# Optimization experiments

Hardware: AMD Instinct MI355X
Metric: run time of the kernel (lower is better)

Reference implementation:

```python
import jax, jax.numpy as jnp
import numpy as np

LAMBDA_COORD = 5.0
LAMBDA_NOOBJ = 0.5
EPS = 1e-16


def setup_inputs() -> dict:
    key = jax.random.key(0)
    k1, k2, k3 = jax.random.split(key, 3)
    B, HW, C = 64, 6400, 85  # 80x80 grid, 5 + 80 classes
    T = 50                   # objects per image
    predictions = jax.random.normal(k1, (B, HW, C), dtype=jnp.float32)
    targets_box = jax.random.uniform(k2, (B, T, 4), dtype=jnp.float32)  # cx, cy, w, h in [0,1)
    targets_cls = jax.random.randint(k3, (B, T), 0, 80)
    return {
        "predictions": predictions,
        "targets_box": targets_box,
        "targets_cls": targets_cls,
        "grid_h": 80,
        "grid_w": 80,
    }


def reference(predictions, targets_box, targets_cls, grid_h, grid_w):
    B, HW, C = predictions.shape
    T = targets_box.shape[1]
    H, W = grid_h, grid_w

    cx, cy, w, h = (targets_box[..., i] for i in range(4))  # each [B, T]
    gxf = jnp.floor(cx * W)
    gyf = jnp.floor(cy * H)
    gi = (gyf * W + gxf).astype(jnp.int32)  # [B, T] grid cell index

    # gather predictions at assigned cells -> [B, T, C]
    g = jnp.take_along_axis(predictions, gi[:, :, None], axis=1)

    # coordinate losses (per-object mean over the 2 components, as F.mse_loss does)
    txy = jnp.stack([cx * W - gxf, cy * H - gyf], axis=-1)           # [B, T, 2]
    xy_loss = jnp.mean((jax.nn.sigmoid(g[..., :2]) - txy) ** 2, -1)  # [B, T]
    twh = jnp.log(jnp.stack([w * W, h * H], axis=-1) + EPS)
    wh_loss = jnp.mean((g[..., 2:4] - twh) ** 2, -1)

    # objectness BCE with target 1: -log(sigmoid(p)) = softplus(-p)
    conf_loss = jax.nn.softplus(-g[..., 4])

    # class cross-entropy
    logp = jax.nn.log_softmax(g[..., 5:], axis=-1)
    cls_loss = -jnp.take_along_axis(logp, targets_cls[..., None], axis=-1)[..., 0]

    per_obj = LAMBDA_COORD * (xy_loss + wh_loss) + conf_loss + cls_loss
    obj_sum = jnp.sum(per_obj)

    # no-object loss: mean BCE(sigmoid(conf), 0) = softplus(p) over cells without objects
    obj_mask = jnp.zeros((B, HW), dtype=bool).at[jnp.arange(B)[:, None], gi].set(True)
    noobj = ~obj_mask
    sp = jax.nn.softplus(predictions[..., 4])  # [B, HW]
    noobj_per_img = jnp.sum(sp * noobj, -1) / jnp.maximum(jnp.sum(noobj, -1), 1)
    noobj_sum = LAMBDA_NOOBJ * jnp.sum(noobj_per_img)

    num_objects = B * T  # all targets are in-grid by construction
    return (obj_sum + noobj_sum) / num_objects
```

## Files before the change

kernel.cpp:

```cpp
#include <hip/hip_runtime.h>
#include <math.h>

constexpr int B_  = 64;
constexpr int HW_ = 6400;
constexpr int C_  = 85;
constexpr int T_  = 50;
constexpr int H_  = 80;
constexpr int W_  = 80;
constexpr float LC    = 5.0f;
constexpr float LN    = 0.5f;
constexpr float INV_N = 1.0f / (B_ * T_);

constexpr int GRID_A = 1600;
constexpr int NPART  = GRID_A + B_ * T_;

__device__ __forceinline__ float softplus_f(float x) {
    return fmaxf(x, 0.0f) + log1pf(expf(-fabsf(x)));
}

__global__ __launch_bounds__(256) void main_kernel(
    const float* __restrict__ pred, const float* __restrict__ tbox,
    const int* __restrict__ tcls, float* __restrict__ partial)
{
    int lane = threadIdx.x & 63;
    int wid  = threadIdx.x >> 6;
    int gw   = blockIdx.x * 4 + wid;
    int bi   = gw / 100;
    int wi   = gw % 100;
    __shared__ float ss[4];

    int cell = wi * 64 + lane;
    float conf = pred[((size_t)bi * HW_ + cell) * C_ + 4];

    int gio;
    if (lane < T_) {
        const float4 to = ((const float4*)tbox)[bi * T_ + lane];
        gio = (int)(floorf(to.y * (float)H_) * (float)W_ +
                    floorf(to.x * (float)W_));
    } else {
        gio = 0x40000000 + lane;
    }
    bool dup = false;
    #pragma unroll
    for (int k = 0; k < T_ - 1; ++k) {
        int gk = __shfl(gio, k, 64);
        dup = dup || ((lane > k) && (gio == gk));
    }
    unsigned long long dm = __ballot(dup);
    int n_unique = T_ - __popcll(dm);
    float nn = fmaxf((float)(HW_ - n_unique), 1.0f);

    float s = softplus_f(conf);
    #pragma unroll
    for (int off = 32; off; off >>= 1) s += __shfl_xor(s, off, 64);
    if (lane == 0) ss[wid] = s;

    if (wi < T_) {
        int obj = bi * T_ + wi;
        int gi  = __shfl(gio, wi, 64);
        bool canonical = !((dm >> wi) & 1ULL);

        const float4 tb = ((const float4*)tbox)[obj];
        float gxf = floorf(tb.x * (float)W_);
        float gyf = floorf(tb.y * (float)H_);

        const float* g = pred + ((size_t)bi * HW_ + gi) * C_;
        int cls = tcls[obj];

        int   c2 = lane + 64;
        float v1 = g[lane];
        float v2 = (c2 < C_) ? g[c2] : 0.0f;

        float m = -1e30f;
        if (lane >= 5) m = v1;
        if (c2 < C_)   m = fmaxf(m, v2);
        #pragma unroll
        for (int off = 32; off; off >>= 1) m = fmaxf(m, __shfl_xor(m, off, 64));
        float e = 0.0f;
        if (lane >= 5) e += expf(v1 - m);
        if (c2 < C_)   e += expf(v2 - m);
        #pragma unroll
        for (int off = 32; off; off >>= 1) e += __shfl_xor(e, off, 64);
        float lse = m + logf(e);

        float contrib = 0.0f;
        if (lane == 0) {
            float d = 1.0f / (1.0f + expf(-v1)) - (tb.x * (float)W_ - gxf);
            contrib = LC * 0.5f * d * d;
        } else if (lane == 1) {
            float d = 1.0f / (1.0f + expf(-v1)) - (tb.y * (float)H_ - gyf);
            contrib = LC * 0.5f * d * d;
        } else if (lane == 2) {
            float d = v1 - logf(tb.z * (float)W_ + 1e-16f);
            contrib = LC * 0.5f * d * d;
        } else if (lane == 3) {
            float d = v1 - logf(tb.w * (float)H_ + 1e-16f);
            contrib = LC * 0.5f * d * d;
        } else if (lane == 4) {
            contrib = softplus_f(-v1);
            if (canonical) contrib -= LN * softplus_f(v1) / nn;
        }
        if (lane == 5 + cls) contrib += lse - v1;
        if (c2   == 5 + cls) contrib += lse - v2;

        #pragma unroll
        for (int off = 32; off; off >>= 1) contrib += __shfl_xor(contrib, off, 64);
        if (lane == 0) partial[GRID_A + obj] = contrib;
    }

    __syncthreads();
    if (threadIdx.x == 0)
        partial[blockIdx.x] = LN * (ss[0] + ss[1] + ss[2] + ss[3]) / nn;
}

__global__ __launch_bounds__(256) void reduce_kernel(
    const float* __restrict__ partial, float* __restrict__ out)
{
    const float4* p4 = (const float4*)partial;
    float s = 0.0f;
    for (int i = threadIdx.x; i < NPART / 4; i += 256) {
        float4 v = p4[i];
        s += (v.x + v.y) + (v.z + v.w);
    }
    #pragma unroll
    for (int off = 32; off; off >>= 1) s += __shfl_xor(s, off, 64);

    __shared__ float ss[4];
    int wid = threadIdx.x >> 6;
    if ((threadIdx.x & 63) == 0) ss[wid] = s;
    __syncthreads();
    if (threadIdx.x == 0)
        out[0] = (ss[0] + ss[1] + ss[2] + ss[3]) * INV_N;
}

extern "C" void kernel_launch(void* const* d_in, const int* in_sizes, int n_in,
                              void* d_out, int out_size, void* d_ws, size_t ws_size,
                              hipStream_t stream) {
    const float* pred = (const float*)d_in[0];
    const float* tbox = (const float*)d_in[1];
    const int*   tcls = (const int*)d_in[2];
    float* out = (float*)d_out;
    float* partial = (float*)d_ws;

    main_kernel  <<<GRID_A, 256, 0, stream>>>(pred, tbox, tcls, partial);
    reduce_kernel<<<1,      256, 0, stream>>>(partial, out);
}
```

Measured before the change: 23.45 us.

## Split main kernel into separate object-loss and no-object scan block roles

Restructures the grid so the first 800 blocks each handle four objects (one wavefront per object) and the remaining 1024 blocks scan the confidence column, 400 cells per block and two cells per thread. Before, object work ran only on the first 50 wavefronts of each image, which left a tail of load imbalance. Each object wavefront now recomputes the duplicate-cell info for its image, adding redundant shuffle work and tbox reads. Total grid size rises from 1600 to 1824 blocks.

New measurement: 20.29 us. 13.5% less time.

```diff
diff --git a/kernel.cpp b/kernel.cpp
--- a/kernel.cpp
+++ b/kernel.cpp
@@ -11,30 +11,23 @@
 constexpr float LN    = 0.5f;
 constexpr float INV_N = 1.0f / (B_ * T_);
 
-constexpr int GRID_A = 1600;
-constexpr int NPART  = GRID_A + B_ * T_;
+constexpr int OBJ_BLOCKS  = (B_ * T_) / 4;
+constexpr int SUBN        = 16;
+constexpr int SCAN_BLOCKS = B_ * SUBN;
+constexpr int CHUNK       = HW_ / SUBN;
+constexpr int GRID_A      = OBJ_BLOCKS + SCAN_BLOCKS;
+constexpr int NPART       = SCAN_BLOCKS + B_ * T_;
 
 __device__ __forceinline__ float softplus_f(float x) {
     return fmaxf(x, 0.0f) + log1pf(expf(-fabsf(x)));
 }
 
-__global__ __launch_bounds__(256) void main_kernel(
-    const float* __restrict__ pred, const float* __restrict__ tbox,
-    const int* __restrict__ tcls, float* __restrict__ partial)
+__device__ __forceinline__ void image_dup_info(
+    const float* __restrict__ tbox, int b, int lane,
+    unsigned long long& dm, float& nn, int& gio)
 {
-    int lane = threadIdx.x & 63;
-    int wid  = threadIdx.x >> 6;
-    int gw   = blockIdx.x * 4 + wid;
-    int bi   = gw / 100;
-    int wi   = gw % 100;
-    __shared__ float ss[4];
-
-    int cell = wi * 64 + lane;
-    float conf = pred[((size_t)bi * HW_ + cell) * C_ + 4];
-
-    int gio;
     if (lane < T_) {
-        const float4 to = ((const float4*)tbox)[bi * T_ + lane];
+        const float4 to = ((const float4*)tbox)[b * T_ + lane];
         gio = (int)(floorf(to.y * (float)H_) * (float)W_ +
                     floorf(to.x * (float)W_));
     } else {
@@ -46,30 +39,37 @@
         int gk = __shfl(gio, k, 64);
         dup = dup || ((lane > k) && (gio == gk));
     }
-    unsigned long long dm = __ballot(dup);
+    dm = __ballot(dup);
     int n_unique = T_ - __popcll(dm);
-    float nn = fmaxf((float)(HW_ - n_unique), 1.0f);
+    nn = fmaxf((float)(HW_ - n_unique), 1.0f);
+}
 
-    float s = softplus_f(conf);
-    #pragma unroll
-    for (int off = 32; off; off >>= 1) s += __shfl_xor(s, off, 64);
-    if (lane == 0) ss[wid] = s;
+__global__ __launch_bounds__(256) void main_kernel(
+    const float* __restrict__ pred, const float* __restrict__ tbox,
+    const int* __restrict__ tcls, float* __restrict__ partial)
+{
+    int lane = threadIdx.x & 63;
+    int wid  = threadIdx.x >> 6;
 
-    if (wi < T_) {
-        int obj = bi * T_ + wi;
-        int gi  = __shfl(gio, wi, 64);
-        bool canonical = !((dm >> wi) & 1ULL);
+    if (blockIdx.x < OBJ_BLOCKS) {
+        int obj = blockIdx.x * 4 + wid;
+        int b   = obj / T_;
+        int myt = obj % T_;
 
         const float4 tb = ((const float4*)tbox)[obj];
         float gxf = floorf(tb.x * (float)W_);
         float gyf = floorf(tb.y * (float)H_);
+        int gi = (int)(gyf * (float)W_ + gxf);
 
-        const float* g = pred + ((size_t)bi * HW_ + gi) * C_;
-        int cls = tcls[obj];
-
+        const float* g = pred + ((size_t)b * HW_ + gi) * C_;
         int   c2 = lane + 64;
         float v1 = g[lane];
         float v2 = (c2 < C_) ? g[c2] : 0.0f;
+        int cls = tcls[obj];
+
+        unsigned long long dm; float nn; int gio;
+        image_dup_info(tbox, b, lane, dm, nn, gio);
+        bool canonical = !((dm >> myt) & 1ULL);
 
         float m = -1e30f;
         if (lane >= 5) m = v1;
@@ -105,12 +105,33 @@
 
         #pragma unroll
         for (int off = 32; off; off >>= 1) contrib += __shfl_xor(contrib, off, 64);
-        if (lane == 0) partial[GRID_A + obj] = contrib;
+        if (lane == 0) partial[SCAN_BLOCKS + obj] = contrib;
+    } else {
+        int c   = blockIdx.x - OBJ_BLOCKS;
+        int b   = c >> 4;
+        int sub = c & 15;
+        const float* p = pred + (size_t)b * HW_ * C_ + 4;
+
+        int i1 = sub * CHUNK + (int)threadIdx.x;
+        float conf1 = p[(size_t)i1 * C_];
+        float conf2 = 0.0f;
+        bool has2 = threadIdx.x < (CHUNK - 256);
+        if (has2) conf2 = p[(size_t)(i1 + 256) * C_];
+
+        unsigned long long dm; float nn; int gio;
+        image_dup_info(tbox, b, lane, dm, nn, gio);
+
+        float s = softplus_f(conf1);
+        if (has2) s += softplus_f(conf2);
+        #pragma unroll
+        for (int off = 32; off; off >>= 1) s += __shfl_xor(s, off, 64);
+
+        __shared__ float ss[4];
+        if (lane == 0) ss[wid] = s;
+        __syncthreads();
+        if (threadIdx.x == 0)
+            partial[c] = LN * (ss[0] + ss[1] + ss[2] + ss[3]) / nn;
     }
-
-    __syncthreads();
-    if (threadIdx.x == 0)
-        partial[blockIdx.x] = LN * (ss[0] + ss[1] + ss[2] + ss[3]) / nn;
 }
 
 __global__ __launch_bounds__(256) void reduce_kernel(
```
